# Performance work log

Hardware: AMD Instinct MI355X
Metric: run time of the kernel (lower is better)

## Reference

```python
import jax, jax.numpy as jnp
import numpy as np

DIM = 512      # model width
HEADS = 8
DH = DIM // 8  # 64, dim_head = dim // 8 per module init
INNER = HEADS * DH  # 512
M = DIM // 2   # 256 landmarks
L_ITERS = 6    # pinv iterations (nystrom-attention default)
KER = 33       # residual depthwise conv kernel (default)
FF = 4 * DIM   # 2048
SEQ = 8191     # +1 cls -> 8192 = 32 * 256, no padding needed
EPS_LN = 1e-5


def _ln(x, g, b):
    mu = x.mean(-1, keepdims=True)
    var = x.var(-1, keepdims=True)
    return (x - mu) / jnp.sqrt(var + EPS_LN) * g + b


def _pinv(x, iters=L_ITERS):
    # iterative Moore-Penrose pseudoinverse (as in nystrom-attention)
    I = jnp.eye(x.shape[-1], dtype=x.dtype)
    ax = jnp.abs(x)
    z = jnp.swapaxes(x, -1, -2) / (ax.sum(-1).max() * ax.sum(-2).max())
    for _ in range(iters):
        xz = x @ z
        z = 0.25 * z @ (13 * I - xz @ (15 * I - xz @ (7 * I - xz)))
    return z


def _nystrom_attn(x, w_qkv, w_out, b_out, conv_w):
    b, n, _ = x.shape
    pad = (-n) % M
    xp = jnp.pad(x, ((0, 0), (pad, 0), (0, 0)))  # F.pad pads on the LEFT
    npad = n + pad
    qkv = xp @ w_qkv  # [b, npad, 3*inner]
    q, k, v = jnp.split(qkv, 3, axis=-1)
    sh = lambda t: t.reshape(b, npad, HEADS, DH).transpose(0, 2, 1, 3)  # b h n d
    q = sh(q) * (DH ** -0.5)
    k = sh(k)
    v = sh(v)
    l = npad // M  # tokens per landmark
    q_l = q.reshape(b, HEADS, M, l, DH).sum(3) / l  # b h m d
    k_l = k.reshape(b, HEADS, M, l, DH).sum(3) / l
    attn1 = jax.nn.softmax(jnp.einsum('bhid,bhjd->bhij', q, k_l), axis=-1)   # [b,h,n,m]
    attn2 = jax.nn.softmax(jnp.einsum('bhid,bhjd->bhij', q_l, k_l), axis=-1)  # [b,h,m,m]
    attn3 = jax.nn.softmax(jnp.einsum('bhid,bhjd->bhij', q_l, k), axis=-1)   # [b,h,m,n]
    out = (attn1 @ _pinv(attn2)) @ (attn3 @ v)  # [b,h,n,d]
    # residual depthwise conv over the sequence dim of v (groups=heads)
    res = jax.lax.conv_general_dilated(
        v, conv_w, window_strides=(1, 1),
        padding=[(KER // 2, KER // 2), (0, 0)],
        dimension_numbers=('NCHW', 'OIHW', 'NCHW'),
        feature_group_count=HEADS)
    out = out + res
    out = out.transpose(0, 2, 1, 3).reshape(b, npad, INNER) @ w_out + b_out
    return out[:, -n:]


def setup_inputs() -> dict:
    key = jax.random.key(0)
    ks = jax.random.split(key, 8)
    rn = lambda k, shape: (jax.random.normal(k, shape, jnp.float32) * 0.02)
    return {
        'x': jax.random.normal(ks[0], (1, SEQ, DIM), jnp.float32),
        'cls_token': rn(ks[1], (1, 1, DIM)),
        'ln1_g': jnp.ones((DIM,), jnp.float32),
        'ln1_b': jnp.zeros((DIM,), jnp.float32),
        'w_qkv': rn(ks[2], (DIM, 3 * INNER)),
        'w_out': rn(ks[3], (INNER, DIM)),
        'b_out': jnp.zeros((DIM,), jnp.float32),
        'conv_w': rn(ks[4], (HEADS, 1, KER, 1)),
        'ln2_g': jnp.ones((DIM,), jnp.float32),
        'ln2_b': jnp.zeros((DIM,), jnp.float32),
        'w1': rn(ks[5], (DIM, FF)),
        'b1': jnp.zeros((FF,), jnp.float32),
        'w2': rn(ks[6], (FF, DIM)),
        'b2': jnp.zeros((DIM,), jnp.float32),
    }


def reference(x, cls_token, ln1_g, ln1_b, w_qkv, w_out, b_out, conv_w,
              ln2_g, ln2_b, w1, b1, w2, b2):
    # prepend cls token (batch must be 1, matching torch.cat semantics)
    x = jnp.concatenate([cls_token, x], axis=1)  # [1, 8192, dim]
    # Nystromformer layer: prenorm attn + residual, prenorm FF + residual
    x = x + _nystrom_attn(_ln(x, ln1_g, ln1_b), w_qkv, w_out, b_out, conv_w)
    h = _ln(x, ln2_g, ln2_b)
    x = x + (jax.nn.gelu(h @ w1 + b1, approximate=False) @ w2 + b2)
    return (x[:, 0], x[:, 1:])
```

## Files before the change

### kernel.cpp

```cpp
#include <hip/hip_runtime.h>
#include <hip/hip_bf16.h>

typedef __attribute__((ext_vector_type(8))) short short8;
typedef __attribute__((ext_vector_type(4))) short short4v;
typedef __attribute__((ext_vector_type(4))) float f32x4;
typedef __hip_bfloat16 bf;

__device__ __forceinline__ void gl_lds16(const void* g, void* l) {
  __builtin_amdgcn_global_load_lds(
      (const __attribute__((address_space(1))) unsigned int*)g,
      (__attribute__((address_space(3))) unsigned int*)l, 16, 0, 0);
}
__device__ __forceinline__ unsigned short f2b(float f) {
  bf h = __float2bfloat16(f);
  return *reinterpret_cast<unsigned short*>(&h);
}
__device__ __forceinline__ float b2f(unsigned short u) {
  unsigned v = ((unsigned)u) << 16;
  return __uint_as_float(v);
}

__global__ __launch_bounds__(256) void concat_ln_k(const float* __restrict__ x,
    const float* __restrict__ cls, const float* __restrict__ g,
    const float* __restrict__ b, float* __restrict__ A, bf* __restrict__ O)
{
  __shared__ float red[256];
  const long row = blockIdx.x; const int tid = threadIdx.x;
  const float* src = (row == 0) ? cls : (x + (row - 1) * 512);
  float v0 = src[tid], v1 = src[tid + 256];
  A[row * 512 + tid] = v0; A[row * 512 + tid + 256] = v1;
  red[tid] = v0 + v1; __syncthreads();
  for (int s = 128; s > 0; s >>= 1) { if (tid < s) red[tid] += red[tid + s]; __syncthreads(); }
  float mean = red[0] * (1.f / 512.f); __syncthreads();
  float d0 = v0 - mean, d1 = v1 - mean;
  red[tid] = d0 * d0 + d1 * d1; __syncthreads();
  for (int s = 128; s > 0; s >>= 1) { if (tid < s) red[tid] += red[tid + s]; __syncthreads(); }
  float rs = rsqrtf(red[0] * (1.f / 512.f) + 1e-5f);
  O[row * 512 + tid]       = __float2bfloat16(d0 * rs * g[tid] + b[tid]);
  O[row * 512 + tid + 256] = __float2bfloat16(d1 * rs * g[tid + 256] + b[tid + 256]);
}

__global__ __launch_bounds__(256) void ln_bf16_k(const float* __restrict__ X,
    const float* __restrict__ g, const float* __restrict__ b,
    bf* __restrict__ O)
{
  __shared__ float red[256];
  const long row = blockIdx.x; const int tid = threadIdx.x;
  const float* r = X + row * 512;
  float v0 = r[tid], v1 = r[tid + 256];
  red[tid] = v0 + v1; __syncthreads();
  for (int s = 128; s > 0; s >>= 1) { if (tid < s) red[tid] += red[tid + s]; __syncthreads(); }
  float mean = red[0] * (1.f / 512.f); __syncthreads();
  float d0 = v0 - mean, d1 = v1 - mean;
  red[tid] = d0 * d0 + d1 * d1; __syncthreads();
  for (int s = 128; s > 0; s >>= 1) { if (tid < s) red[tid] += red[tid + s]; __syncthreads(); }
  float rs = rsqrtf(red[0] * (1.f / 512.f) + 1e-5f);
  O[row * 512 + tid]       = __float2bfloat16(d0 * rs * g[tid] + b[tid]);
  O[row * 512 + tid + 256] = __float2bfloat16(d1 * rs * g[tid + 256] + b[tid + 256]);
}

__global__ __launch_bounds__(256) void tconv_k(const float* __restrict__ W,
    bf* __restrict__ WT, int K, int N)
{
  __shared__ float t[64][65];
  const int n0 = blockIdx.x << 6, k0 = blockIdx.y << 6;
  const int c = threadIdx.x & 63; const int r4 = threadIdx.x >> 6;
  #pragma unroll 4
  for (int i = 0; i < 16; i++) {
    int r = r4 * 16 + i;
    t[r][c] = W[(long)(k0 + r) * N + n0 + c];
  }
  __syncthreads();
  #pragma unroll 4
  for (int i = 0; i < 16; i++) {
    int r = r4 * 16 + i;
    WT[(long)(n0 + r) * K + k0 + c] = __float2bfloat16(t[c][r]);
  }
}

template<int EPI>
__global__ __launch_bounds__(256) void gemm_bf(
    const bf* __restrict__ Ag, const bf* __restrict__ Bg,
    void* __restrict__ Cg, const float* __restrict__ Res,
    const float* __restrict__ bias, int K, int N,
    bf* __restrict__ Qb, bf* __restrict__ Kb, bf* __restrict__ Vb)
{
  __shared__ __align__(16) short As[2][2][128][32];
  __shared__ __align__(16) short Bs[2][2][128][32];
  const int tid = threadIdx.x, lane = tid & 63, wid = tid >> 6;
  const int nwg = gridDim.x * gridDim.y;
  const int lin = blockIdx.y * gridDim.x + blockIdx.x;
  const int nl = (lin & 7) * (nwg >> 3) + (lin >> 3);
  const int bxi = nl % gridDim.x, byi = nl / gridDim.x;
  const int brow = byi << 7, bcol = bxi << 7;
  const int wr = (wid >> 1) << 6, wc = (wid & 1) << 6;
  const int fr = lane & 15, fs = lane >> 4;
  const int srow = lane >> 2, skp = (lane & 3) << 3;
  f32x4 acc[4][4];
  #pragma unroll
  for (int m = 0; m < 4; m++)
    #pragma unroll
    for (int n = 0; n < 4; n++) acc[m][n] = (f32x4){0.f, 0.f, 0.f, 0.f};

  const bf* Arow = Ag + (long)brow * K;
  const bf* Brow = Bg + (long)bcol * K;

  auto stage = [&](int bufi, int koff) {
    #pragma unroll
    for (int i = 0; i < 4; i++) {
      int c = (wid << 2) + i, rg = c >> 1, hf = c & 1;
      gl_lds16(Arow + (long)(rg * 16 + srow) * K + koff + hf * 32 + skp,
               &As[bufi][hf][rg * 16][0]);
      gl_lds16(Brow + (long)(rg * 16 + srow) * K + koff + hf * 32 + skp,
               &Bs[bufi][hf][rg * 16][0]);
    }
  };

  stage(0, 0);
  __syncthreads();
  const int nk = K >> 6;
  for (int t = 0; t < nk; ++t) {
    const int buf = t & 1;
    if (t + 1 < nk) stage(buf ^ 1, (t + 1) << 6);
    #pragma unroll
    for (int kk = 0; kk < 2; kk++) {
      short8 a[4], b[4];
      #pragma unroll
      for (int m = 0; m < 4; m++)
        a[m] = *(const short8*)&As[buf][kk][wr + m * 16 + fr][fs * 8];
      #pragma unroll
      for (int n = 0; n < 4; n++)
        b[n] = *(const short8*)&Bs[buf][kk][wc + n * 16 + fr][fs * 8];
      #pragma unroll
      for (int m = 0; m < 4; m++)
        #pragma unroll
        for (int n = 0; n < 4; n++)
          acc[m][n] = __builtin_amdgcn_mfma_f32_16x16x32_bf16(a[m], b[n], acc[m][n], 0, 0, 0);
    }
    __syncthreads();
  }

  #pragma unroll
  for (int m = 0; m < 4; m++) {
    #pragma unroll
    for (int n = 0; n < 4; n++) {
      const int col = bcol + wc + n * 16 + fr;
      #pragma unroll
      for (int j = 0; j < 4; j++) {
        const long row = brow + wr + m * 16 + fs * 4 + j;
        float v = acc[m][n][j];
        if (EPI == 1) {
          v += bias[col] + Res[row * N + col];
          ((float*)Cg)[row * N + col] = v;
        } else if (EPI == 2) {
          v += bias[col];
          v = 0.5f * v * (1.f + erff(v * 0.70710678118654752f));
          ((bf*)Cg)[row * N + col] = __float2bfloat16(v);
        } else {
          int sect = col >> 9, h = (col >> 6) & 7, d = col & 63;
          long o = ((long)h * 8192 + row) * 64 + d;
          if (sect == 0)      Qb[o] = __float2bfloat16(v * 0.125f);
          else if (sect == 1) Kb[o] = __float2bfloat16(v);
          else                Vb[o] = __float2bfloat16(v);
        }
      }
    }
  }
}

template<int CS, int DIAG>
__global__ __launch_bounds__(256) void pgemm_k(
    const bf* __restrict__ Ag, const bf* __restrict__ Bg,
    bf* __restrict__ Cg, bf* __restrict__ Tg, float alpha, float s)
{
  __shared__ __align__(16) short As[8][64][32];
  __shared__ __align__(16) short Bs[8][64][32];
  short (*Tt)[68] = (short(*)[68])&As[0][0][0];
  const int tid = threadIdx.x, lane = tid & 63, wid = tid >> 6;
  const int lin = (blockIdx.z * 4 + blockIdx.y) * 4 + blockIdx.x;
  const int nl = (lin & 7) * 16 + (lin >> 3);
  const int bz = nl >> 4, rem = nl & 15;
  const long base = (long)bz << 16;
  const int brow = (rem >> 2) << 6, bcol = (rem & 3) << 6;
  const int wr = (wid >> 1) << 5, wc = (wid & 1) << 5;
  const int fr = lane & 15, fs = lane >> 4;
  const int srow = lane >> 2, skp = (lane & 3) << 3;
  const bf* Arow = Ag + base + (long)brow * 256;
  const bf* Brow = Bg + base + (long)bcol * 256;
  #pragma unroll
  for (int i = 0; i < 16; i++) {
    int c = (wid << 4) + i;
    int mat = c >> 5, c5 = c & 31, rg = c5 >> 3, ks = c5 & 7;
    const bf* src = (mat ? Brow : Arow) + (long)(rg * 16 + srow) * 256 + ks * 32 + skp;
    gl_lds16(src, mat ? &Bs[ks][rg * 16][0] : &As[ks][rg * 16][0]);
  }
  __syncthreads();
  f32x4 acc[2][2];
  #pragma unroll
  for (int m = 0; m < 2; m++)
    #pragma unroll
    for (int n = 0; n < 2; n++) acc[m][n] = (f32x4){0.f, 0.f, 0.f, 0.f};
  #pragma unroll
  for (int ks = 0; ks < 8; ks++) {
    short8 a[2], b[2];
    #pragma unroll
    for (int m = 0; m < 2; m++)
      a[m] = *(const short8*)&As[ks][wr + m * 16 + fr][fs * 8];
    #pragma unroll
    for (int n = 0; n < 2; n++)
      b[n] = *(const short8*)&Bs[ks][wc + n * 16 + fr][fs * 8];
    #pragma unroll
    for (int m = 0; m < 2; m++)
      #pragma unroll
      for (int n = 0; n < 2; n++)
        acc[m][n] = __builtin_amdgcn_mfma_f32_16x16x32_bf16(a[m], b[n], acc[m][n], 0, 0, 0);
  }
  if (CS) {
    #pragma unroll
    for (int m = 0; m < 2; m++)
      #pragma unroll
      for (int n = 0; n < 2; n++) {
        const int col = bcol + wc + n * 16 + fr;
        #pragma unroll
        for (int j = 0; j < 4; j++)
          (Cg + base)[(long)(brow + wr + m * 16 + fs * 4 + j) * 256 + col] =
              __float2bfloat16(acc[m][n][j] * alpha);
      }
  }
  __syncthreads();
  #pragma unroll
  for (int m = 0; m < 2; m++)
    #pragma unroll
    for (int n = 0; n < 2; n++) {
      const int lcol = wc + n * 16 + fr;
      #pragma unroll
      for (int j = 0; j < 4; j++) {
        const int lrow = wr + m * 16 + fs * 4 + j;
        float v = acc[m][n][j] * alpha;
        float o = DIAG ? (((brow + lrow) == (bcol + lcol)) ? (s - v) : (-v)) : v;
        Tt[lcol][lrow] = (short)f2b(o);
      }
    }
  __syncthreads();
  {
    const int lcol = tid >> 2, q = tid & 3;
    short8 w0 = *(const short8*)&Tt[lcol][q * 16];
    short8 w1 = *(const short8*)&Tt[lcol][q * 16 + 8];
    bf* dst = Tg + base + (long)(bcol + lcol) * 256 + brow + q * 16;
    *(short8*)dst = w0;
    *(short8*)(dst + 8) = w1;
  }
}

template<int EPI>
__global__ __launch_bounds__(256) void bgemm(
    const bf* __restrict__ Ag, const bf* __restrict__ Bg,
    void* __restrict__ Cg, bf* __restrict__ Tg,
    int Nc, float alpha, float s,
    long lda, long ldb, long ldc, long ldt,
    long sA, long sB, long sC, long sT)
{
  __shared__ __align__(16) short As[2][2][128][32];
  __shared__ __align__(16) short Bs[2][2][128][32];
  const int tid = threadIdx.x, lane = tid & 63, wid = tid >> 6;
  const int hh = blockIdx.z;
  const int brow = blockIdx.y << 7, bcol = blockIdx.x << 7;
  const int wr = (wid >> 1) << 6, wc = (wid & 1) << 6;
  const int fr = lane & 15, fs = lane >> 4;
  const int srow = lane >> 2, skp = (lane & 3) << 3;
  f32x4 acc[4][4];
  #pragma unroll
  for (int m = 0; m < 4; m++)
    #pragma unroll
    for (int n = 0; n < 4; n++) acc[m][n] = (f32x4){0.f, 0.f, 0.f, 0.f};

  const bf* Arow = Ag + hh * sA + (long)brow * lda;
  const bf* Brow = Bg + hh * sB + (long)bcol * ldb;

  auto stage = [&](int bufi, int koff) {
    #pragma unroll
    for (int i = 0; i < 4; i++) {
      int c = (wid << 2) + i, rg = c >> 1, hf = c & 1;
      gl_lds16(Arow + (long)(rg * 16 + srow) * lda + koff + hf * 32 + skp,
               &As[bufi][hf][rg * 16][0]);
      gl_lds16(Brow + (long)(rg * 16 + srow) * ldb + koff + hf * 32 + skp,
               &Bs[bufi][hf][rg * 16][0]);
    }
  };

  stage(0, 0);
  __syncthreads();
  #pragma unroll
  for (int t = 0; t < 4; ++t) {
    const int buf = t & 1;
    if (t < 3) stage(buf ^ 1, (t + 1) << 6);
    #pragma unroll
    for (int kk = 0; kk < 2; kk++) {
      short8 a[4], b[4];
      #pragma unroll
      for (int m = 0; m < 4; m++)
        a[m] = *(const short8*)&As[buf][kk][wr + m * 16 + fr][fs * 8];
      #pragma unroll
      for (int n = 0; n < 4; n++)
        b[n] = *(const short8*)&Bs[buf][kk][wc + n * 16 + fr][fs * 8];
      #pragma unroll
      for (int m = 0; m < 4; m++)
        #pragma unroll
        for (int n = 0; n < 4; n++)
          acc[m][n] = __builtin_amdgcn_mfma_f32_16x16x32_bf16(a[m], b[n], acc[m][n], 0, 0, 0);
    }
    __syncthreads();
  }

  #pragma unroll
  for (int m = 0; m < 4; m++) {
    #pragma unroll
    for (int n = 0; n < 4; n++) {
      const int col = bcol + wc + n * 16 + fr;
      const int rbase = brow + wr + m * 16 + fs * 4;
      if (EPI != 6 || col < Nc) {
        bf* Tb = Tg + hh * sT;
        short4v tv;
        #pragma unroll
        for (int j = 0; j < 4; j++) tv[j] = (short)f2b(acc[m][n][j] * alpha);
        *(short4v*)&Tb[(long)col * ldt + rbase] = tv;
      }
    }
  }
}

__global__ __launch_bounds__(256) void sgemm_k(
    const float* __restrict__ A, const float* __restrict__ Bw,
    float* __restrict__ C,
    int K, long lda, long ldb, long ldc,
    long sA, long sB, long sC)
{
  __shared__ float As[16][68];
  __shared__ __align__(16) float Bs[16][68];
  const int tid = threadIdx.x;
  const int zz = blockIdx.z;
  const float* Ab = A + zz * sA;
  const float* Bb = Bw + zz * sB;
  float* Cb = C + zz * sC;
  const int brow = blockIdx.y * 64;
  const int bcol = blockIdx.x * 64;
  const int tm = tid >> 4, tn = tid & 15;
  const int lam = tid >> 2;
  const int lak = (tid & 3) << 2;
  const int lbk = tid >> 4;
  const int lbn = (tid & 15) << 2;
  float acc[4][4];
  #pragma unroll
  for (int i = 0; i < 4; i++)
    #pragma unroll
    for (int j = 0; j < 4; j++) acc[i][j] = 0.f;

  for (int k0 = 0; k0 < K; k0 += 16) {
    float4 av = *(const float4*)&Ab[(long)(brow + lam) * lda + k0 + lak];
    As[lak + 0][lam] = av.x; As[lak + 1][lam] = av.y;
    As[lak + 2][lam] = av.z; As[lak + 3][lam] = av.w;
    float4 bv = *(const float4*)&Bb[(long)(k0 + lbk) * ldb + bcol + lbn];
    *(float4*)&Bs[lbk][lbn] = bv;
    __syncthreads();
    #pragma unroll
    for (int kk = 0; kk < 16; kk++) {
      float a0 = As[kk][(tm << 2) + 0], a1 = As[kk][(tm << 2) + 1];
      float a2 = As[kk][(tm << 2) + 2], a3 = As[kk][(tm << 2) + 3];
      float b0 = Bs[kk][(tn << 2) + 0], b1 = Bs[kk][(tn << 2) + 1];
      float b2 = Bs[kk][(tn << 2) + 2], b3 = Bs[kk][(tn << 2) + 3];
      acc[0][0] += a0 * b0; acc[0][1] += a0 * b1; acc[0][2] += a0 * b2; acc[0][3] += a0 * b3;
      acc[1][0] += a1 * b0; acc[1][1] += a1 * b1; acc[1][2] += a1 * b2; acc[1][3] += a1 * b3;
      acc[2][0] += a2 * b0; acc[2][1] += a2 * b1; acc[2][2] += a2 * b2; acc[2][3] += a2 * b3;
      acc[3][0] += a3 * b0; acc[3][1] += a3 * b1; acc[3][2] += a3 * b2; acc[3][3] += a3 * b3;
    }
    __syncthreads();
  }
  #pragma unroll
  for (int i = 0; i < 4; i++) {
    const long row = brow + (tm << 2) + i;
    #pragma unroll
    for (int j = 0; j < 4; j++) {
      const int col = bcol + (tn << 2) + j;
      Cb[row * ldc + col] = acc[i][j];
    }
  }
}

__global__ __launch_bounds__(256) void landmarks_k(const bf* __restrict__ Qb,
    const bf* __restrict__ Kb,
    float* __restrict__ QL, float* __restrict__ KLT,
    bf* __restrict__ QLb, bf* __restrict__ KLb)
{
  int t = blockIdx.x * 256 + threadIdx.x;
  int d = t & 63; int m = (t >> 6) & 255; int h = t >> 14;
  const unsigned short* qp = (const unsigned short*)Qb + ((long)h * 8192 + m * 32) * 64 + d;
  const unsigned short* kp = (const unsigned short*)Kb + ((long)h * 8192 + m * 32) * 64 + d;
  float sq = 0.f, sk = 0.f;
  for (int i = 0; i < 32; i++) { sq += b2f(qp[i * 64]); sk += b2f(kp[i * 64]); }
  float qv = sq * (1.f / 32.f);
  QL[t] = qv;
  QLb[t] = __float2bfloat16(qv);
  float kv = sk * (1.f / 32.f);
  KLb[t] = __float2bfloat16(kv);
  KLT[(h << 14) + (d << 8) + m] = kv;
}

__global__ __launch_bounds__(256) void vt_k(const bf* __restrict__ Vb,
    bf* __restrict__ VT)
{
  __shared__ unsigned short t[64][68];
  const int h = blockIdx.x & 7; const int n0 = (blockIdx.x >> 3) << 6;
  const int c = threadIdx.x & 63; const int r4 = threadIdx.x >> 6;
  const unsigned short* vp = (const unsigned short*)Vb;
  unsigned short* vo = (unsigned short*)VT;
  #pragma unroll 4
  for (int i = 0; i < 16; i++) {
    int r = r4 * 16 + i;
    t[r][c] = vp[((long)h * 8192 + n0 + r) * 64 + c];
  }
  __syncthreads();
  #pragma unroll 4
  for (int i = 0; i < 16; i++) {
    int d = r4 * 16 + i;
    vo[((long)(h << 6) + d) * 8192 + n0 + c] = t[c][d];
  }
}

__global__ __launch_bounds__(256) void softmax256_k(float* __restrict__ X)
{
  __shared__ float red[256];
  const long row = blockIdx.x; const int tid = threadIdx.x;
  float v = X[row * 256 + tid];
  red[tid] = v; __syncthreads();
  for (int s = 128; s > 0; s >>= 1) { if (tid < s) red[tid] = fmaxf(red[tid], red[tid + s]); __syncthreads(); }
  float M = red[0]; __syncthreads();
  float e = __expf(v - M);
  red[tid] = e; __syncthreads();
  for (int s = 128; s > 0; s >>= 1) { if (tid < s) red[tid] += red[tid + s]; __syncthreads(); }
  float S = red[0];
  X[row * 256 + tid] = e / S;
}

__global__ __launch_bounds__(256) void colsum_k(const float* __restrict__ X, float* __restrict__ out)
{
  int t = blockIdx.x * 256 + threadIdx.x; int h = t >> 8; int j = t & 255;
  const float* c = X + ((long)h << 16) + j;
  float s = 0.f;
  for (int i = 0; i < 256; i++) s += fabsf(c[(long)i << 8]);
  out[t] = s;
}
__global__ __launch_bounds__(256) void invscale_k(const float* __restrict__ cols,
    float* __restrict__ inv)
{
  __shared__ float red[256];
  int tid = threadIdx.x;
  float mc = -1e30f;
  for (int i = tid; i < 2048; i += 256) mc = fmaxf(mc, cols[i]);
  red[tid] = mc; __syncthreads();
  for (int s = 128; s > 0; s >>= 1) { if (tid < s) red[tid] = fmaxf(red[tid], red[tid + s]); __syncthreads(); }
  if (tid == 0) inv[0] = 1.0f / red[0];
}

__global__ __launch_bounds__(256) void xz_init_k(const float* __restrict__ ATT2,
    const float* __restrict__ inv, bf* __restrict__ Xb,
    bf* __restrict__ z0, bf* __restrict__ z0T)
{
  __shared__ float t[64][65];
  const int h = blockIdx.z;
  const int j0 = blockIdx.x << 6, i0 = blockIdx.y << 6;
  const int c = threadIdx.x & 63; const int r4 = threadIdx.x >> 6;
  const float iv = inv[0];
  #pragma unroll 4
  for (int i = 0; i < 16; i++) {
    int r = r4 * 16 + i;
    float v = ATT2[((long)h << 16) + (long)(i0 + r) * 256 + j0 + c];
    t[r][c] = v;
    Xb[((long)h << 16) + (long)(i0 + r) * 256 + j0 + c]  = __float2bfloat16(v);
    z0T[((long)h << 16) + (long)(i0 + r) * 256 + j0 + c] = __float2bfloat16(v * iv);
  }
  __syncthreads();
  #pragma unroll 4
  for (int i = 0; i < 16; i++) {
    int r = r4 * 16 + i;
    z0[((long)h << 16) + (long)(j0 + r) * 256 + i0 + c] = __float2bfloat16(t[c][r] * iv);
  }
}

__global__ __launch_bounds__(256) void attn3f_k(
    const bf* __restrict__ Qlb, const bf* __restrict__ Kb, const bf* __restrict__ Vt,
    float* __restrict__ Op, float* __restrict__ Mp, float* __restrict__ Lp)
{
  __shared__ __align__(16) short Qs[2][128][32];
  __shared__ __align__(16) short Ks[2][128][32];
  __shared__ __align__(16) short Vs[4][64][32];
  __shared__ __align__(16) short Ps[4][4][32][32];
  const int tid = threadIdx.x, lane = tid & 63, wid = tid >> 6;
  const int fr = lane & 15, fs = lane >> 4;
  const int srow = lane >> 2, skp = (lane & 3) << 3;
  const int lin = (blockIdx.z * 2 + blockIdx.y) * 16 + blockIdx.x;
  const int nl = (lin & 7) * 32 + (lin >> 3);
  const int chunk = nl & 15, mt = (nl >> 4) & 1, h = nl >> 5;
  const int wrb = wid << 5;
  const bf* Qg = Qlb + ((long)h * 256 + mt * 128) * 64;
  #pragma unroll
  for (int i = 0; i < 4; i++) {
    int c = (wid << 2) + i, rg = c >> 1, hf = c & 1;
    gl_lds16(Qg + (long)(rg * 16 + srow) * 64 + hf * 32 + skp, &Qs[hf][rg * 16][0]);
  }
  f32x4 acc2[2][4];
  float mrun[2][4], lrun[2][4];
  #pragma unroll
  for (int m = 0; m < 2; m++)
    #pragma unroll
    for (int n = 0; n < 4; n++) { acc2[m][n] = (f32x4){0.f,0.f,0.f,0.f}; mrun[m][n] = -1e30f; lrun[m][n] = 0.f; }

  for (int t = 0; t < 4; t++) {
    const int key0 = (chunk << 9) + (t << 7);
    const bf* Kg = Kb + ((long)h * 8192 + key0) * 64;
    #pragma unroll
    for (int i = 0; i < 4; i++) {
      int c = (wid << 2) + i, rg = c >> 1, hf = c & 1;
      gl_lds16(Kg + (long)(rg * 16 + srow) * 64 + hf * 32 + skp, &Ks[hf][rg * 16][0]);
    }
    #pragma unroll
    for (int i = 0; i < 4; i++) {
      int c = (wid << 2) + i, dg = c >> 2, ks = c & 3;
      gl_lds16(Vt + ((long)h * 64 + dg * 16 + srow) * 8192 + key0 + ks * 32 + skp,
               &Vs[ks][dg * 16][0]);
    }
    __syncthreads();
    f32x4 lac[2][8];
    #pragma unroll
    for (int m = 0; m < 2; m++)
      #pragma unroll
      for (int n = 0; n < 8; n++) lac[m][n] = (f32x4){0.f,0.f,0.f,0.f};
    #pragma unroll
    for (int kk = 0; kk < 2; kk++) {
      short8 a[2];
      #pragma unroll
      for (int m = 0; m < 2; m++)
        a[m] = *(const short8*)&Qs[kk][wrb + m * 16 + fr][fs * 8];
      #pragma unroll
      for (int n = 0; n < 8; n++) {
        short8 b = *(const short8*)&Ks[kk][n * 16 + fr][fs * 8];
        #pragma unroll
        for (int m = 0; m < 2; m++)
          lac[m][n] = __builtin_amdgcn_mfma_f32_16x16x32_bf16(a[m], b, lac[m][n], 0, 0, 0);
      }
    }
    #pragma unroll
    for (int m = 0; m < 2; m++) {
      #pragma unroll
      for (int j = 0; j < 4; j++) {
        float tmax = lac[m][0][j];
        #pragma unroll
        for (int n = 1; n < 8; n++) tmax = fmaxf(tmax, lac[m][n][j]);
        tmax = fmaxf(tmax, __shfl_xor(tmax, 1));
        tmax = fmaxf(tmax, __shfl_xor(tmax, 2));
        tmax = fmaxf(tmax, __shfl_xor(tmax, 4));
        tmax = fmaxf(tmax, __shfl_xor(tmax, 8));
        float mnew = fmaxf(mrun[m][j], tmax);
        float sc = __expf(mrun[m][j] - mnew);
        #pragma unroll
        for (int n2 = 0; n2 < 4; n2++) acc2[m][n2][j] *= sc;
        float lsum = 0.f;
        #pragma unroll
        for (int n = 0; n < 8; n++) {
          float p = __expf(lac[m][n][j] - mnew);
          lac[m][n][j] = p; lsum += p;
        }
        lsum += __shfl_xor(lsum, 1);
        lsum += __shfl_xor(lsum, 2);
        lsum += __shfl_xor(lsum, 4);
        lsum += __shfl_xor(lsum, 8);
        lrun[m][j] = lrun[m][j] * sc + lsum;
        mrun[m][j] = mnew;
      }
    }
    #pragma unroll
    for (int m = 0; m < 2; m++)
      #pragma unroll
      for (int n = 0; n < 8; n++) {
        int col = n * 16 + fr;
        #pragma unroll
        for (int j = 0; j < 4; j++)
          Ps[wid][col >> 5][m * 16 + fs * 4 + j][col & 31] = (short)f2b(lac[m][n][j]);
      }
    #pragma unroll
    for (int ks = 0; ks < 4; ks++) {
      short8 a2[2];
      #pragma unroll
      for (int m = 0; m < 2; m++)
        a2[m] = *(const short8*)&Ps[wid][ks][m * 16 + fr][fs * 8];
      #pragma unroll
      for (int n = 0; n < 4; n++) {
        short8 b2 = *(const short8*)&Vs[ks][n * 16 + fr][fs * 8];
        #pragma unroll
        for (int m = 0; m < 2; m++)
          acc2[m][n] = __builtin_amdgcn_mfma_f32_16x16x32_bf16(a2[m], b2, acc2[m][n], 0, 0, 0);
      }
    }
    __syncthreads();
  }
  const long base = (long)(chunk * 8 + h) * 2 + mt;
  #pragma unroll
  for (int m = 0; m < 2; m++)
    #pragma unroll
    for (int n = 0; n < 4; n++) {
      int col = n * 16 + fr;
      #pragma unroll
      for (int j = 0; j < 4; j++)
        Op[base * 8192 + (long)(wrb + m * 16 + fs * 4 + j) * 64 + col] = acc2[m][n][j];
    }
  if (fr == 0) {
    #pragma unroll
    for (int m = 0; m < 2; m++)
      #pragma unroll
      for (int j = 0; j < 4; j++) {
        int r = wrb + m * 16 + fs * 4 + j;
        Mp[base * 128 + r] = mrun[m][j];
        Lp[base * 128 + r] = lrun[m][j];
      }
  }
}

__global__ __launch_bounds__(256) void attn3c_k(
    const float* __restrict__ Op, const float* __restrict__ Mp,
    const float* __restrict__ Lp, bf* __restrict__ AVT)
{
  __shared__ float wm[16][16];
  __shared__ float wl[16][16];
  const int bid = blockIdx.x;
  const int h = bid >> 4, mt = (bid >> 3) & 1, rs = bid & 7;
  const int tid = threadIdx.x;
  const int r0 = rs * 16;
  {
    int c = tid >> 4, r = tid & 15;
    long idx = ((long)(c * 8 + h) * 2 + mt) * 128 + r0 + r;
    wm[c][r] = Mp[idx];
    wl[c][r] = Lp[idx];
  }
  __syncthreads();
  if (tid < 16) {
    int r = tid;
    float M = wm[0][r];
    #pragma unroll
    for (int c = 1; c < 16; c++) M = fmaxf(M, wm[c][r]);
    float D = 0.f;
    #pragma unroll
    for (int c = 0; c < 16; c++) D += __expf(wm[c][r] - M) * wl[c][r];
    float rv = 1.0f / D;
    #pragma unroll
    for (int c = 0; c < 16; c++) wm[c][r] = __expf(wm[c][r] - M) * rv;
  }
  __syncthreads();
  #pragma unroll
  for (int i = 0; i < 4; i++) {
    int idx = i * 256 + tid;
    int r = idx >> 6, d = idx & 63;
    float s = 0.f;
    #pragma unroll
    for (int c = 0; c < 16; c++)
      s += wm[c][r] * Op[((long)(c * 8 + h) * 2 + mt) * 8192 + (long)(r0 + r) * 64 + d];
    AVT[(long)h * 16384 + d * 256 + mt * 128 + r0 + r] = __float2bfloat16(s);
  }
}

__global__ __launch_bounds__(256) void attn1_k(
    const bf* __restrict__ Qb, const bf* __restrict__ KLb,
    const bf* __restrict__ CMT, bf* __restrict__ Bhb)
{
  __shared__ __align__(16) char U[65536];
  short (*As)[128][32] = (short(*)[128][32])U;
  short (*Bs)[256][32] = (short(*)[256][32])(U + 16384);
  short (*Ps)[128][32] = (short(*)[128][32])U;
  __shared__ __align__(16) short Cs[8][64][32];
  __shared__ float red[2][2][128];

  const int tid = threadIdx.x;
  const int lane = tid & 63, wid = tid >> 6;
  const int fr = lane & 15, fs = lane >> 4;
  const int srow = lane >> 2, skp = (lane & 3) << 3;
  const int n0 = blockIdx.x << 7, h = blockIdx.y;
  const int half = wid & 1, wrb = (wid >> 1) << 6;

  const bf* Aq = Qb  + (long)h * 524288 + (long)n0 * 64;
  const bf* Bk = KLb + (long)h * 16384;
  const bf* Cm = CMT + (long)h * 16384;

  for (int i = 0; i < 20; i++) {
    int c = wid * 20 + i;
    if (c < 16) {
      int rg = c >> 1, hf = c & 1;
      gl_lds16(Aq + (long)(rg * 16 + srow) * 64 + hf * 32 + skp, &As[hf][rg * 16][0]);
    } else if (c < 48) {
      int c2 = c - 16; int rg = c2 >> 1, hf = c2 & 1;
      gl_lds16(Bk + (long)(rg * 16 + srow) * 64 + hf * 32 + skp, &Bs[hf][rg * 16][0]);
    } else {
      int c3 = c - 48; int rg = c3 >> 3, ks = c3 & 7;
      gl_lds16(Cm + (long)(rg * 16 + srow) * 256 + ks * 32 + skp, &Cs[ks][rg * 16][0]);
    }
  }
  __syncthreads();

  f32x4 acc[4][8];
  #pragma unroll
  for (int m = 0; m < 4; m++)
    #pragma unroll
    for (int n = 0; n < 8; n++) acc[m][n] = (f32x4){0.f, 0.f, 0.f, 0.f};
  #pragma unroll
  for (int kk = 0; kk < 2; kk++) {
    short8 a[4];
    #pragma unroll
    for (int m = 0; m < 4; m++)
      a[m] = *(const short8*)&As[kk][wrb + m * 16 + fr][fs * 8];
    #pragma unroll
    for (int n = 0; n < 8; n++) {
      short8 b = *(const short8*)&Bs[kk][half * 128 + n * 16 + fr][fs * 8];
      #pragma unroll
      for (int m = 0; m < 4; m++)
        acc[m][n] = __builtin_amdgcn_mfma_f32_16x16x32_bf16(a[m], b, acc[m][n], 0, 0, 0);
    }
  }

  #pragma unroll
  for (int m = 0; m < 4; m++)
    #pragma unroll
    for (int j = 0; j < 4; j++) {
      float mx = -1e30f;
      #pragma unroll
      for (int n = 0; n < 8; n++) mx = fmaxf(mx, acc[m][n][j]);
      mx = fmaxf(mx, __shfl_xor(mx, 1));
      mx = fmaxf(mx, __shfl_xor(mx, 2));
      mx = fmaxf(mx, __shfl_xor(mx, 4));
      mx = fmaxf(mx, __shfl_xor(mx, 8));
      int rloc = wrb + m * 16 + fs * 4 + j;
      if (fr == 0) red[0][half][rloc] = mx;
    }
  __syncthreads();
  #pragma unroll
  for (int m = 0; m < 4; m++)
    #pragma unroll
    for (int j = 0; j < 4; j++) {
      int rloc = wrb + m * 16 + fs * 4 + j;
      float Mx = fmaxf(red[0][0][rloc], red[0][1][rloc]);
      float s = 0.f;
      #pragma unroll
      for (int n = 0; n < 8; n++) {
        float e = __expf(acc[m][n][j] - Mx);
        acc[m][n][j] = e; s += e;
      }
      s += __shfl_xor(s, 1);
      s += __shfl_xor(s, 2);
      s += __shfl_xor(s, 4);
      s += __shfl_xor(s, 8);
      if (fr == 0) red[1][half][rloc] = s;
    }
  __syncthreads();
  #pragma unroll
  for (int m = 0; m < 4; m++)
    #pragma unroll
    for (int j = 0; j < 4; j++) {
      int rloc = wrb + m * 16 + fs * 4 + j;
      float inv = 1.0f / (red[1][0][rloc] + red[1][1][rloc]);
      #pragma unroll
      for (int n = 0; n < 8; n++) {
        int col = half * 128 + n * 16 + fr;
        Ps[col >> 5][rloc][col & 31] = (short)f2b(acc[m][n][j] * inv);
      }
    }
  __syncthreads();

  f32x4 acc2[4][2];
  #pragma unroll
  for (int m = 0; m < 4; m++)
    #pragma unroll
    for (int n = 0; n < 2; n++) acc2[m][n] = (f32x4){0.f, 0.f, 0.f, 0.f};
  const int wc2 = half * 32;
  #pragma unroll
  for (int kk = 0; kk < 8; kk++) {
    short8 a2[4];
    #pragma unroll
    for (int m = 0; m < 4; m++)
      a2[m] = *(const short8*)&Ps[kk][wrb + m * 16 + fr][fs * 8];
    #pragma unroll
    for (int n = 0; n < 2; n++) {
      short8 b2 = *(const short8*)&Cs[kk][wc2 + n * 16 + fr][fs * 8];
      #pragma unroll
      for (int m = 0; m < 4; m++)
        acc2[m][n] = __builtin_amdgcn_mfma_f32_16x16x32_bf16(a2[m], b2, acc2[m][n], 0, 0, 0);
    }
  }
  #pragma unroll
  for (int m = 0; m < 4; m++)
    #pragma unroll
    for (int n = 0; n < 2; n++) {
      int col = wc2 + n * 16 + fr;
      #pragma unroll
      for (int j = 0; j < 4; j++) {
        long row = n0 + wrb + m * 16 + fs * 4 + j;
        Bhb[row * 512 + h * 64 + col] = __float2bfloat16(acc2[m][n][j]);
      }
    }
}

__global__ __launch_bounds__(256) void convres_k(const bf* __restrict__ Vb,
    const float* __restrict__ W, bf* __restrict__ Bhb)
{
  const int gid = blockIdx.x * 256 + threadIdx.x;
  const int n = gid >> 7, q = gid & 127;
  const int j0 = q << 2, h = j0 >> 6, d0 = j0 & 63;
  float a0 = 0.f, a1 = 0.f, a2 = 0.f, a3 = 0.f;
  const unsigned short* vb = (const unsigned short*)Vb + (long)h * 524288 + d0;
  #pragma unroll
  for (int kk = 0; kk < 33; kk++) {
    int nn = n + kk - 16;
    if (nn >= 0 && nn < 8192) {
      float w = W[h * 33 + kk];
      uint2 raw = *(const uint2*)(vb + (long)nn * 64);
      a0 += w * b2f(raw.x & 0xffff); a1 += w * b2f(raw.x >> 16);
      a2 += w * b2f(raw.y & 0xffff); a3 += w * b2f(raw.y >> 16);
    }
  }
  unsigned short* o = (unsigned short*)Bhb + (long)n * 512 + j0;
  uint2 cur = *(uint2*)o;
  uint2 outv;
  outv.x = (unsigned)f2b(b2f(cur.x & 0xffff) + a0) | ((unsigned)f2b(b2f(cur.x >> 16) + a1) << 16);
  outv.y = (unsigned)f2b(b2f(cur.y & 0xffff) + a2) | ((unsigned)f2b(b2f(cur.y >> 16) + a3) << 16);
  *(uint2*)o = outv;
}

extern "C" void kernel_launch(void* const* d_in, const int* in_sizes, int n_in,
                              void* d_out, int out_size, void* d_ws, size_t ws_size,
                              hipStream_t stream)
{
  const float* x     = (const float*)d_in[0];
  const float* cls   = (const float*)d_in[1];
  const float* ln1g  = (const float*)d_in[2];
  const float* ln1b  = (const float*)d_in[3];
  const float* wqkv  = (const float*)d_in[4];
  const float* wout  = (const float*)d_in[5];
  const float* bout  = (const float*)d_in[6];
  const float* convw = (const float*)d_in[7];
  const float* ln2g  = (const float*)d_in[8];
  const float* ln2b  = (const float*)d_in[9];
  const float* w1    = (const float*)d_in[10];
  const float* b1    = (const float*)d_in[11];
  const float* w2    = (const float*)d_in[12];
  const float* b2    = (const float*)d_in[13];
  float* out = (float*)d_out;
  float* ws  = (float*)d_ws;

  float* A     = ws + 0;
  float* QL    = ws + 4194304;
  float* KLT   = ws + 4325376;
  float* ATT2  = ws + 4456448;
  float* csum  = ws + 4980736;
  float* inv   = ws + 4982784;
  float* Opart = ws + 4982800;
  float* Mpart = ws + 7079952;
  float* Lpart = ws + 7112720;
  bf* Qbf  = (bf*)(ws + 7145488);
  bf* Kbf  = (bf*)(ws + 9242640);
  bf* Vbf  = (bf*)(ws + 11339792);
  bf* VT   = (bf*)(ws + 13436944);
  bf* QLbf = (bf*)(ws + 15534096);
  bf* KLbf = (bf*)(ws + 15599632);
  bf* Xbf  = (bf*)(ws + 15665168);
  bf* zA   = (bf*)(ws + 15927312);
  bf* zAT  = (bf*)(ws + 16189456);
  bf* zB   = (bf*)(ws + 16451600);
  bf* zBT  = (bf*)(ws + 16713744);
  bf* Gbf  = (bf*)(ws + 16975888);
  bf* TB0  = (bf*)(ws + 17238032);
  bf* TB1  = (bf*)(ws + 17500176);
  bf* AVT  = (bf*)(ws + 17762320);
  bf* CMT  = (bf*)(ws + 17827856);
  float* R = ws + 17893392;
  bf* wqkvT = (bf*)R;
  bf* ln1bf = (bf*)(R + 393216);
  bf* Bhbf  = (bf*)(R + 393216);
  bf* FF1bf = (bf*)R;
  bf* w1T   = Kbf;
  bf* w2T   = Kbf + 1048576;
  bf* woutT = Kbf + 2097152;
  bf* ln2bf = VT;

  concat_ln_k<<<8192, 256, 0, stream>>>(x, cls, ln1g, ln1b, A, ln1bf);
  tconv_k<<<dim3(24, 8), 256, 0, stream>>>(wqkv, wqkvT, 512, 1536);
  gemm_bf<3><<<dim3(12, 64), 256, 0, stream>>>(ln1bf, wqkvT, nullptr, nullptr, nullptr,
      512, 1536, Qbf, Kbf, Vbf);
  landmarks_k<<<512, 256, 0, stream>>>(Qbf, Kbf, QL, KLT, QLbf, KLbf);
  vt_k<<<1024, 256, 0, stream>>>(Vbf, VT);
  sgemm_k<<<dim3(4, 4, 8), 256, 0, stream>>>(QL, KLT, ATT2,
      64, 64, 256, 256, 16384, 16384, 65536);
  softmax256_k<<<2048, 256, 0, stream>>>(ATT2);
  colsum_k<<<8, 256, 0, stream>>>(ATT2, csum);
  invscale_k<<<1, 256, 0, stream>>>(csum, inv);
  xz_init_k<<<dim3(4, 4, 8), 256, 0, stream>>>(ATT2, inv, Xbf, zA, zAT);
  {
    bf* zc = zA; bf* zcT = zAT; bf* zn = zB; bf* znT = zBT;
    for (int it = 0; it < 6; ++it) {
      pgemm_k<1,1><<<dim3(4, 4, 8), 256, 0, stream>>>(Xbf, zcT, Gbf, TB0, 1.f, 7.f);
      pgemm_k<0,1><<<dim3(4, 4, 8), 256, 0, stream>>>(Gbf, TB0, nullptr, TB1, 1.f, 15.f);
      pgemm_k<0,1><<<dim3(4, 4, 8), 256, 0, stream>>>(Gbf, TB1, nullptr, TB0, 1.f, 13.f);
      pgemm_k<1,0><<<dim3(4, 4, 8), 256, 0, stream>>>(zc, TB0, zn, znT, 0.25f, 0.f);
      bf* t = zc; zc = zn; zn = t; t = zcT; zcT = znT; znT = t;
    }
  }
  attn3f_k<<<dim3(16, 2, 8), 256, 0, stream>>>(QLbf, Kbf, VT, Opart, Mpart, Lpart);
  attn3c_k<<<128, 256, 0, stream>>>(Opart, Mpart, Lpart, AVT);
  bgemm<6><<<dim3(1, 2, 8), 256, 0, stream>>>(zA, AVT, nullptr, CMT,
      64, 1.f, 0.f, 256, 256, 0, 256, 65536, 16384, 0, 16384);
  tconv_k<<<dim3(32, 8), 256, 0, stream>>>(w1, w1T, 512, 2048);
  tconv_k<<<dim3(8, 32), 256, 0, stream>>>(w2, w2T, 2048, 512);
  tconv_k<<<dim3(8, 8), 256, 0, stream>>>(wout, woutT, 512, 512);
  attn1_k<<<dim3(64, 8), 256, 0, stream>>>(Qbf, KLbf, CMT, Bhbf);
  convres_k<<<4096, 256, 0, stream>>>(Vbf, convw, Bhbf);
  gemm_bf<1><<<dim3(4, 64), 256, 0, stream>>>(Bhbf, woutT, A, A, bout, 512, 512,
      nullptr, nullptr, nullptr);
  ln_bf16_k<<<8192, 256, 0, stream>>>(A, ln2g, ln2b, ln2bf);
  gemm_bf<2><<<dim3(16, 64), 256, 0, stream>>>(ln2bf, w1T, FF1bf, nullptr, b1, 512, 2048,
      nullptr, nullptr, nullptr);
  gemm_bf<1><<<dim3(4, 64), 256, 0, stream>>>(FF1bf, w2T, out, A, b2, 2048, 512,
      nullptr, nullptr, nullptr);
}
```

Baseline: 457.0 us.

## Enlarge bf16 GEMM tiles to 256x256 with 512 threads and dynamic LDS

```diff
diff --git a/kernel.cpp b/kernel.cpp
--- a/kernel.cpp
+++ b/kernel.cpp
@@ -79,26 +79,25 @@
 }
 
 template<int EPI>
-__global__ __launch_bounds__(256) void gemm_bf(
+__global__ __launch_bounds__(512) void gemm256(
     const bf* __restrict__ Ag, const bf* __restrict__ Bg,
     void* __restrict__ Cg, const float* __restrict__ Res,
     const float* __restrict__ bias, int K, int N,
     bf* __restrict__ Qb, bf* __restrict__ Kb, bf* __restrict__ Vb)
 {
-  __shared__ __align__(16) short As[2][2][128][32];
-  __shared__ __align__(16) short Bs[2][2][128][32];
+  extern __shared__ short LDS[];
   const int tid = threadIdx.x, lane = tid & 63, wid = tid >> 6;
   const int nwg = gridDim.x * gridDim.y;
   const int lin = blockIdx.y * gridDim.x + blockIdx.x;
   const int nl = (lin & 7) * (nwg >> 3) + (lin >> 3);
   const int bxi = nl % gridDim.x, byi = nl / gridDim.x;
-  const int brow = byi << 7, bcol = bxi << 7;
-  const int wr = (wid >> 1) << 6, wc = (wid & 1) << 6;
+  const int brow = byi << 8, bcol = bxi << 8;
+  const int wr2 = (wid >> 2) << 7, wc2 = (wid & 3) << 6;
   const int fr = lane & 15, fs = lane >> 4;
   const int srow = lane >> 2, skp = (lane & 3) << 3;
-  f32x4 acc[4][4];
-  #pragma unroll
-  for (int m = 0; m < 4; m++)
+  f32x4 acc[8][4];
+  #pragma unroll
+  for (int m = 0; m < 8; m++)
     #pragma unroll
     for (int n = 0; n < 4; n++) acc[m][n] = (f32x4){0.f, 0.f, 0.f, 0.f};
 
@@ -106,13 +105,14 @@
   const bf* Brow = Bg + (long)bcol * K;
 
   auto stage = [&](int bufi, int koff) {
-    #pragma unroll
-    for (int i = 0; i < 4; i++) {
-      int c = (wid << 2) + i, rg = c >> 1, hf = c & 1;
-      gl_lds16(Arow + (long)(rg * 16 + srow) * K + koff + hf * 32 + skp,
-               &As[bufi][hf][rg * 16][0]);
-      gl_lds16(Brow + (long)(rg * 16 + srow) * K + koff + hf * 32 + skp,
-               &Bs[bufi][hf][rg * 16][0]);
+    short* base = LDS + bufi * 32768;
+    #pragma unroll
+    for (int i = 0; i < 8; i++) {
+      int c = (wid << 3) + i;
+      int mat = c >> 5, c5 = c & 31, rg = c5 >> 1, hf = c5 & 1;
+      const bf* src = (mat ? Brow : Arow)
+          + (long)(rg * 16 + srow) * K + koff + hf * 32 + skp;
+      gl_lds16(src, base + mat * 16384 + hf * 8192 + rg * 512);
     }
   };
 
@@ -122,32 +122,33 @@
   for (int t = 0; t < nk; ++t) {
     const int buf = t & 1;
     if (t + 1 < nk) stage(buf ^ 1, (t + 1) << 6);
+    const short* Ab = LDS + buf * 32768;
+    const short* Bb = Ab + 16384;
     #pragma unroll
     for (int kk = 0; kk < 2; kk++) {
-      short8 a[4], b[4];
-      #pragma unroll
-      for (int m = 0; m < 4; m++)
-        a[m] = *(const short8*)&As[buf][kk][wr + m * 16 + fr][fs * 8];
-      #pragma unroll
-      for (int n = 0; n < 4; n++)
-        b[n] = *(const short8*)&Bs[buf][kk][wc + n * 16 + fr][fs * 8];
-      #pragma unroll
-      for (int m = 0; m < 4; m++)
+      short8 a[8];
+      #pragma unroll
+      for (int m = 0; m < 8; m++)
+        a[m] = *(const short8*)&Ab[kk * 8192 + (wr2 + m * 16 + fr) * 32 + fs * 8];
+      #pragma unroll
+      for (int n = 0; n < 4; n++) {
+        short8 b = *(const short8*)&Bb[kk * 8192 + (wc2 + n * 16 + fr) * 32 + fs * 8];
         #pragma unroll
-        for (int n = 0; n < 4; n++)
-          acc[m][n] = __builtin_amdgcn_mfma_f32_16x16x32_bf16(a[m], b[n], acc[m][n], 0, 0, 0);
+        for (int m = 0; m < 8; m++)
+          acc[m][n] = __builtin_amdgcn_mfma_f32_16x16x32_bf16(a[m], b, acc[m][n], 0, 0, 0);
+      }
     }
     __syncthreads();
   }
 
   #pragma unroll
-  for (int m = 0; m < 4; m++) {
+  for (int m = 0; m < 8; m++) {
     #pragma unroll
     for (int n = 0; n < 4; n++) {
-      const int col = bcol + wc + n * 16 + fr;
+      const int col = bcol + wc2 + n * 16 + fr;
       #pragma unroll
       for (int j = 0; j < 4; j++) {
-        const long row = brow + wr + m * 16 + fs * 4 + j;
+        const long row = brow + wr2 + m * 16 + fs * 4 + j;
         float v = acc[m][n][j];
         if (EPI == 1) {
           v += bias[col] + Res[row * N + col];
@@ -850,6 +851,11 @@
   const float* b2    = (const float*)d_in[13];
   float* out = (float*)d_out;
   float* ws  = (float*)d_ws;
+
+  const int DLDS = 131072;
+  hipFuncSetAttribute((const void*)gemm256<1>, hipFuncAttributeMaxDynamicSharedMemorySize, DLDS);
+  hipFuncSetAttribute((const void*)gemm256<2>, hipFuncAttributeMaxDynamicSharedMemorySize, DLDS);
+  hipFuncSetAttribute((const void*)gemm256<3>, hipFuncAttributeMaxDynamicSharedMemorySize, DLDS);
 
   float* A     = ws + 0;
   float* QL    = ws + 4194304;
@@ -888,7 +894,7 @@
 
   concat_ln_k<<<8192, 256, 0, stream>>>(x, cls, ln1g, ln1b, A, ln1bf);
   tconv_k<<<dim3(24, 8), 256, 0, stream>>>(wqkv, wqkvT, 512, 1536);
-  gemm_bf<3><<<dim3(12, 64), 256, 0, stream>>>(ln1bf, wqkvT, nullptr, nullptr, nullptr,
+  gemm256<3><<<dim3(6, 32), 512, DLDS, stream>>>(ln1bf, wqkvT, nullptr, nullptr, nullptr,
       512, 1536, Qbf, Kbf, Vbf);
   landmarks_k<<<512, 256, 0, stream>>>(Qbf, Kbf, QL, KLT, QLbf, KLbf);
   vt_k<<<1024, 256, 0, stream>>>(Vbf, VT);
@@ -917,11 +923,11 @@
   tconv_k<<<dim3(8, 8), 256, 0, stream>>>(wout, woutT, 512, 512);
   attn1_k<<<dim3(64, 8), 256, 0, stream>>>(Qbf, KLbf, CMT, Bhbf);
   convres_k<<<4096, 256, 0, stream>>>(Vbf, convw, Bhbf);
-  gemm_bf<1><<<dim3(4, 64), 256, 0, stream>>>(Bhbf, woutT, A, A, bout, 512, 512,
+  gemm256<1><<<dim3(2, 32), 512, DLDS, stream>>>(Bhbf, woutT, A, A, bout, 512, 512,
       nullptr, nullptr, nullptr);
   ln_bf16_k<<<8192, 256, 0, stream>>>(A, ln2g, ln2b, ln2bf);
-  gemm_bf<2><<<dim3(16, 64), 256, 0, stream>>>(ln2bf, w1T, FF1bf, nullptr, b1, 512, 2048,
+  gemm256<2><<<dim3(8, 32), 512, DLDS, stream>>>(ln2bf, w1T, FF1bf, nullptr, b1, 512, 2048,
       nullptr, nullptr, nullptr);
-  gemm_bf<1><<<dim3(4, 64), 256, 0, stream>>>(FF1bf, w2T, out, A, b2, 2048, 512,
+  gemm256<1><<<dim3(2, 32), 512, DLDS, stream>>>(FF1bf, w2T, out, A, b2, 2048, 512,
       nullptr, nullptr, nullptr);
 }
```

Result: slower. 506.4 us (+10.8%).
